# Kernel tuning notes

Hardware: AMD Instinct MI355X
Metric: run time of the kernel (lower is better)

Reference implementation:

```python
import jax, jax.numpy as jnp
import numpy as np

BITS = 4
MAXQ = (1 << BITS) - 1  # 15
PACK = 32 // BITS       # 8 nibbles per int32


def setup_inputs() -> dict:
    key = jax.random.key(0)
    k = jax.random.split(key, 6)
    B, S, IN, OUT, G = 4, 2048, 4096, 4096, 32
    groups = IN // G  # 128
    imin, imax = np.iinfo(np.int32).min, np.iinfo(np.int32).max
    x = jax.random.normal(k[0], (B, S, IN), dtype=jnp.float32)
    qweight = jax.random.randint(k[1], (IN // PACK, OUT), imin, imax, dtype=jnp.int32)
    qzeros = jax.random.randint(k[2], (groups, OUT // PACK), imin, imax, dtype=jnp.int32)
    qscales = jax.random.randint(k[3], (groups, OUT, 1), 0, 256, dtype=jnp.int32)
    qscales_zeros = jax.random.uniform(k[4], (groups, 1, 1), dtype=jnp.float32)
    qscales_scales = jax.random.uniform(k[5], (groups, 1, 1), dtype=jnp.float32) * 0.01
    g_idx = (jnp.arange(IN, dtype=jnp.int32) // G)
    return {"x": x, "qweight": qweight, "qzeros": qzeros, "qscales": qscales,
            "qscales_zeros": qscales_zeros, "qscales_scales": qscales_scales, "g_idx": g_idx}


def reference(x, qweight, qzeros, qscales, qscales_zeros, qscales_scales, g_idx):
    out_features = qweight.shape[-1]
    shifts = jnp.arange(0, 32, BITS, dtype=jnp.int32)  # (8,)
    # --- unpack int4 weights: (in/8, 8, out) -> (in, out); mask makes arith shift == logical
    w = (qweight[:, None, :] >> shifts[None, :, None]) & MAXQ
    w = w.reshape(-1, out_features)  # (in, out), values 0..15
    # --- unpack zeros: (groups, out/8, 8) -> (groups, out); +1 per original
    z = ((qzeros[:, :, None] >> shifts[None, None, :]) & MAXQ) + 1
    z = z.reshape(qzeros.shape[0], -1)  # (groups, out)
    z = z[g_idx]  # (in, out)
    # --- double-dequant scales: (groups, out, 1) with (groups, 1, 1) stats
    scales = (qscales.astype(x.dtype) - qscales_zeros) * qscales_scales
    scales = scales.reshape(qscales.shape[0], -1)[g_idx]  # (in, out)
    weight = ((w - z) * scales).astype(x.dtype)  # (in, out)
    return jnp.matmul(x, weight)
```

## Files before the change

kernel.cpp:

```cpp
#include <hip/hip_runtime.h>

typedef __attribute__((ext_vector_type(8))) short short8;
typedef __attribute__((ext_vector_type(4))) float floatx4;
typedef unsigned int u32;
typedef unsigned short u16;

__device__ __forceinline__ u16 f2bf(float f) {
  u32 u = __float_as_uint(f);
  u += 0x7FFFu + ((u >> 16) & 1u);
  return (u16)(u >> 16);
}

typedef const __attribute__((address_space(1))) u32* gp1_t;
typedef __attribute__((address_space(3))) u32* lp3_t;

__device__ __forceinline__ void gld16(const void* g, void* l) {
  __builtin_amdgcn_global_load_lds((gp1_t)g, (lp3_t)l, 16, 0, 0);
}

__global__ __launch_bounds__(256) void xconv(const float* __restrict__ x,
                                             u16* __restrict__ xb, long long n4) {
  long long i = (long long)blockIdx.x * 256 + threadIdx.x;
  if (i >= n4) return;
  float4 v = ((const float4*)x)[i];
  ushort4 o;
  o.x = f2bf(v.x); o.y = f2bf(v.y); o.z = f2bf(v.z); o.w = f2bf(v.w);
  ((ushort4*)xb)[i] = o;
}

__global__ __launch_bounds__(256) void dequant(
    const int* __restrict__ qw, const int* __restrict__ qz,
    const int* __restrict__ qs, const float* __restrict__ qsz,
    const float* __restrict__ qss, const int* __restrict__ gidx,
    u16* __restrict__ Wt, int IN, int OUT) {
  const int n = blockIdx.x * 64 + (threadIdx.x & 63);
  const int w = threadIdx.x >> 6;
  const int k0 = blockIdx.y * 128 + w * 32;
  const int g = gidx[k0];
  const int kk0 = k0 >> 3;
  const int zq = ((qz[(size_t)g * (OUT >> 3) + (n >> 3)] >> (4 * (n & 7))) & 15) + 1;
  const float sc = ((float)qs[(size_t)g * OUT + n] - qsz[g]) * qss[g];
  u16* dst = Wt + (size_t)n * IN + k0;
#pragma unroll
  for (int j = 0; j < 4; ++j) {
    const int w32 = qw[(size_t)(kk0 + j) * OUT + n];
    u16 o[8];
#pragma unroll
    for (int s = 0; s < 8; ++s)
      o[s] = f2bf((float)(((w32 >> (4 * s)) & 15) - zq) * sc);
    uint4 pk;
    pk.x = (u32)o[0] | ((u32)o[1] << 16);
    pk.y = (u32)o[2] | ((u32)o[3] << 16);
    pk.z = (u32)o[4] | ((u32)o[5] << 16);
    pk.w = (u32)o[6] | ((u32)o[7] << 16);
    *(uint4*)(dst + j * 8) = pk;
  }
}

#define VM4 asm volatile("s_waitcnt vmcnt(4)" ::: "memory")
#define VM0 asm volatile("s_waitcnt vmcnt(0)" ::: "memory")

__global__ __launch_bounds__(512, 2) void gemm256(const u16* __restrict__ A,
                                                  const u16* __restrict__ Bt,
                                                  float* __restrict__ C,
                                                  int M, int N, int K) {
  __shared__ u16 As[2][16384];
  __shared__ u16 Bs[2][16384];
  const int tid = threadIdx.x;
  const int lane = tid & 63;
  const int wave = tid >> 6;
  const int wm = wave >> 2;
  const int wn = wave & 3;
  const int lr = lane & 15, quad = lane >> 4;

  const int nbx = N >> 8;
  const int nwg = gridDim.x;
  const int bid = blockIdx.x;
  const int q8 = nwg >> 3, r8 = nwg & 7;
  const int xcd = bid & 7, loc = bid >> 3;
  const int swz = (xcd < r8 ? xcd * (q8 + 1) : r8 * (q8 + 1) + (xcd - r8) * q8) + loc;
  const int n0 = (swz % nbx) << 8;
  const int m0 = (swz / nbx) << 8;

  floatx4 acc[8][4] = {};

  const int srow = lane >> 3;
  const int sch8 = ((lane & 7) ^ (srow & 7)) * 8;
  const u16* aS = A + (size_t)(m0 + wave * 8 + srow) * K + sch8;
  const u16* bS = Bt + (size_t)(n0 + wave * 8 + srow) * K + sch8;

#define STAGE_A(buf, h, kt) do {                                              \
    const u16* s_ = aS + (size_t)(h) * 128 * K + (size_t)(kt) * 64;           \
    u16* d_ = &As[buf][((h) * 128 + wave * 8) * 64];                          \
    gld16(s_, d_); gld16(s_ + (size_t)64 * K, d_ + 4096);                     \
  } while (0)
#define STAGE_B(buf, h, kt) do {                                              \
    const u16* s_ = bS + (size_t)(h) * 128 * K + (size_t)(kt) * 64;           \
    u16* d_ = &Bs[buf][((h) * 128 + wave * 8) * 64];                          \
    gld16(s_, d_); gld16(s_ + (size_t)64 * K, d_ + 4096);                     \
  } while (0)

  const int rl = lr & 7;
  const int cs0 = ((0 * 4 + quad) ^ rl) * 8;
  const int cs1 = ((1 * 4 + quad) ^ rl) * 8;
  const u16* a0rd = &As[0][(wm * 128 + lr) * 64];
  const u16* a1rd = &As[1][(wm * 128 + lr) * 64];
  const u16* b0rd = &Bs[0][(wn * 64 + lr) * 64];
  const u16* b1rd = &Bs[1][(wn * 64 + lr) * 64];

  short8 aF[2][2], bF[4][2];

#define PHASE(ARD, BRD, q, LOADB, STG, VMW) do {                              \
    if (LOADB) {                                                              \
      _Pragma("unroll") for (int nt = 0; nt < 4; ++nt) {                      \
        bF[nt][0] = *(const short8*)((BRD) + nt * 1024 + cs0);                \
        bF[nt][1] = *(const short8*)((BRD) + nt * 1024 + cs1);                \
      }                                                                       \
    }                                                                         \
    aF[0][0] = *(const short8*)((ARD) + (2 * (q)) * 1024 + cs0);              \
    aF[0][1] = *(const short8*)((ARD) + (2 * (q)) * 1024 + cs1);              \
    aF[1][0] = *(const short8*)((ARD) + (2 * (q) + 1) * 1024 + cs0);          \
    aF[1][1] = *(const short8*)((ARD) + (2 * (q) + 1) * 1024 + cs1);          \
    STG;                                                                      \
    __builtin_amdgcn_s_barrier();                                             \
    __builtin_amdgcn_s_setprio(1);                                            \
    _Pragma("unroll") for (int s = 0; s < 2; ++s)                             \
      _Pragma("unroll") for (int j = 0; j < 2; ++j)                           \
        _Pragma("unroll") for (int nt = 0; nt < 4; ++nt)                      \
          acc[2 * (q) + j][nt] = __builtin_amdgcn_mfma_f32_16x16x32_bf16(     \
              aF[j][s], bF[nt][s], acc[2 * (q) + j][nt], 0, 0, 0);            \
    __builtin_amdgcn_s_setprio(0);                                            \
    VMW;                                                                      \
    __builtin_amdgcn_s_barrier();                                             \
  } while (0)

  STAGE_B(0, 0, 0); STAGE_B(0, 1, 0);
  STAGE_A(0, 0, 0); STAGE_A(0, 1, 0);
  STAGE_B(1, 0, 1); STAGE_B(1, 1, 1);
  VM4;
  __builtin_amdgcn_s_barrier();

  const int NI = K >> 7;
  for (int i = 0; i < NI; ++i) {
    const int kt = 2 * i;
    const bool full = (i < NI - 1);
    PHASE(a0rd, b0rd, 0, 1, { STAGE_A(1, 0, kt + 1); }, (void)0);
    PHASE(a0rd, b0rd, 1, 0, { STAGE_A(1, 1, kt + 1); }, (void)0);
    PHASE(a0rd, b0rd, 2, 0, { if (full) STAGE_B(0, 0, kt + 2); }, (void)0);
    PHASE(a0rd, b0rd, 3, 0, { if (full) STAGE_B(0, 1, kt + 2); },
          { if (full) { VM4; } else { VM0; } });
    PHASE(a1rd, b1rd, 0, 1, { if (full) STAGE_A(0, 0, kt + 2); }, (void)0);
    PHASE(a1rd, b1rd, 1, 0, { if (full) STAGE_A(0, 1, kt + 2); }, (void)0);
    PHASE(a1rd, b1rd, 2, 0, { if (full) STAGE_B(1, 0, kt + 3); }, (void)0);
    PHASE(a1rd, b1rd, 3, 0, { if (full) STAGE_B(1, 1, kt + 3); },
          { if (full) { VM4; } });
  }
#undef PHASE
#undef STAGE_A
#undef STAGE_B

#pragma unroll
  for (int mt = 0; mt < 8; ++mt)
#pragma unroll
    for (int nt = 0; nt < 4; ++nt)
#pragma unroll
      for (int r = 0; r < 4; ++r) {
        int row = m0 + wm * 128 + mt * 16 + quad * 4 + r;
        int col = n0 + wn * 64 + nt * 16 + lr;
        C[(size_t)row * N + col] = acc[mt][nt][r];
      }
}

__global__ __launch_bounds__(256) void gemm(const u16* __restrict__ A,
                                            const u16* __restrict__ Bt,
                                            float* __restrict__ C,
                                            int M, int N, int K) {
  __shared__ u16 As[128 * 64];
  __shared__ u16 Bs[128 * 64];
  const int tid = threadIdx.x;
  const int lane = tid & 63;
  const int wave = tid >> 6;
  const int wm = wave & 1, wn = wave >> 1;
  const int lr = lane & 15, quad = lane >> 4;
  const int m0 = blockIdx.y * 128, n0 = blockIdx.x * 128;

  floatx4 acc[4][4] = {};

  const int srowB = (lane >> 3);
  const int schunk = (lane & 7) ^ srowB;
  const int rowA0 = wave * 32;
  const u16* aSrc = A + (size_t)(m0 + rowA0 + srowB) * K + schunk * 8;
  const u16* bSrc = Bt + (size_t)(n0 + rowA0 + srowB) * K + schunk * 8;
  u16* aDst = &As[rowA0 * 64];
  u16* bDst = &Bs[rowA0 * 64];
  const size_t rstep = (size_t)8 * K;

  const int rx = lr & 7;

  for (int k0 = 0; k0 < K; k0 += 64) {
    __syncthreads();
#pragma unroll
    for (int c = 0; c < 4; ++c) {
      gld16(aSrc + c * rstep + k0, aDst + c * 8 * 64);
      gld16(bSrc + c * rstep + k0, bDst + c * 8 * 64);
    }
    __syncthreads();

#pragma unroll
    for (int h = 0; h < 2; ++h) {
      short8 aF[4], bF[4];
      const int rc = ((quad + 4 * h) ^ rx) * 8;
#pragma unroll
      for (int t = 0; t < 4; ++t) {
        aF[t] = *(const short8*)&As[(wm * 64 + t * 16 + lr) * 64 + rc];
        bF[t] = *(const short8*)&Bs[(wn * 64 + t * 16 + lr) * 64 + rc];
      }
#pragma unroll
      for (int mt = 0; mt < 4; ++mt)
#pragma unroll
        for (int nt = 0; nt < 4; ++nt)
          acc[mt][nt] = __builtin_amdgcn_mfma_f32_16x16x32_bf16(
              aF[mt], bF[nt], acc[mt][nt], 0, 0, 0);
    }
  }

#pragma unroll
  for (int mt = 0; mt < 4; ++mt)
#pragma unroll
    for (int nt = 0; nt < 4; ++nt)
#pragma unroll
      for (int r = 0; r < 4; ++r) {
        int row = m0 + wm * 64 + mt * 16 + quad * 4 + r;
        int col = n0 + wn * 64 + nt * 16 + lr;
        C[(size_t)row * N + col] = acc[mt][nt][r];
      }
}

__global__ void naive(const float* __restrict__ x, const int* __restrict__ qw,
                      const int* __restrict__ qz, const int* __restrict__ qs,
                      const float* __restrict__ qsz, const float* __restrict__ qss,
                      const int* __restrict__ gidx, float* __restrict__ out,
                      int M, int N, int K) {
  int n = blockIdx.x * 64 + (threadIdx.x & 63);
  int m = blockIdx.y * 4 + (threadIdx.x >> 6);
  if (n >= N || m >= M) return;
  float acc = 0.f;
  for (int kk = 0; kk < K / 8; ++kk) {
    int w32 = qw[(size_t)kk * N + n];
#pragma unroll
    for (int s = 0; s < 8; ++s) {
      int k = kk * 8 + s;
      int g = gidx[k];
      int zq = ((qz[(size_t)g * (N >> 3) + (n >> 3)] >> (4 * (n & 7))) & 15) + 1;
      float sc = ((float)qs[(size_t)g * N + n] - qsz[g]) * qss[g];
      acc += x[(size_t)m * K + k] * ((float)((w32 >> (4 * s)) & 15) - (float)zq) * sc;
    }
  }
  out[(size_t)m * N + n] = acc;
}

extern "C" void kernel_launch(void* const* d_in, const int* in_sizes, int n_in,
                              void* d_out, int out_size, void* d_ws, size_t ws_size,
                              hipStream_t stream) {
  const float* x = (const float*)d_in[0];
  const int* qw = (const int*)d_in[1];
  const int* qz = (const int*)d_in[2];
  const int* qs = (const int*)d_in[3];
  const float* qsz = (const float*)d_in[4];
  const float* qss = (const float*)d_in[5];
  const int* gidx = (const int*)d_in[6];
  const int IN = in_sizes[6];
  const int OUT = (int)(((long long)in_sizes[1] * 8) / IN);
  const int M = in_sizes[0] / IN;
  float* out = (float*)d_out;

  size_t bytesW = (size_t)IN * OUT * 2;
  size_t bytesX = (size_t)M * IN * 2;
  bool haveWs = (ws_size >= bytesW + bytesX);
  bool fast256 = haveWs && (M % 256 == 0) && (OUT % 256 == 0) &&
                 (IN % 128 == 0) && (IN >= 256);
  bool fast128 = haveWs && (M % 128 == 0) && (OUT % 128 == 0) && (IN % 128 == 0);

  if (fast256 || fast128) {
    u16* Wt = (u16*)d_ws;
    u16* Xb = (u16*)((char*)d_ws + bytesW);
    long long n4 = (long long)M * IN / 4;
    int cb = (int)((n4 + 255) / 256);
    xconv<<<cb, 256, 0, stream>>>(x, Xb, n4);
    dequant<<<dim3(OUT / 64, IN / 128), 256, 0, stream>>>(qw, qz, qs, qsz, qss,
                                                          gidx, Wt, IN, OUT);
    if (fast256) {
      int nblk = (M / 256) * (OUT / 256);
      gemm256<<<dim3(nblk), 512, 0, stream>>>(Xb, Wt, out, M, OUT, IN);
    } else {
      gemm<<<dim3(OUT / 128, M / 128), 256, 0, stream>>>(Xb, Wt, out, M, OUT, IN);
    }
  } else {
    naive<<<dim3((OUT + 63) / 64, (M + 3) / 4), 256, 0, stream>>>(
        x, qw, qz, qs, qsz, qss, gidx, out, M, OUT, IN);
  }
}
```

Before: 489.8 us.

## Restructure GEMM main loop into two-barrier tiles and coalesce dequant stores via LDS

The GEMM main loop is rewritten from eight single-barrier phases per iteration into per-k-tile blocks. Each block waits on vmcnt once, loads all B and low A fragments, issues the next A stage, runs MFMAs while loading the high A fragments, then barriers and issues the next B stage. This aims to cut barrier count and overlap LDS reads with MFMA, at the cost of more live registers and a peeled epilogue. The dequant kernel now stages its output through shared memory so global stores of the transposed weight are coalesced, and xconv becomes a grid-stride loop capped at 2048 blocks.

```diff
diff --git a/kernel.cpp b/kernel.cpp
--- a/kernel.cpp
+++ b/kernel.cpp
@@ -20,12 +20,13 @@
 
 __global__ __launch_bounds__(256) void xconv(const float* __restrict__ x,
                                              u16* __restrict__ xb, long long n4) {
-  long long i = (long long)blockIdx.x * 256 + threadIdx.x;
-  if (i >= n4) return;
-  float4 v = ((const float4*)x)[i];
-  ushort4 o;
-  o.x = f2bf(v.x); o.y = f2bf(v.y); o.z = f2bf(v.z); o.w = f2bf(v.w);
-  ((ushort4*)xb)[i] = o;
+  const long long stride = (long long)gridDim.x * 256;
+  for (long long i = (long long)blockIdx.x * 256 + threadIdx.x; i < n4; i += stride) {
+    float4 v = ((const float4*)x)[i];
+    ushort4 o;
+    o.x = f2bf(v.x); o.y = f2bf(v.y); o.z = f2bf(v.z); o.w = f2bf(v.w);
+    ((ushort4*)xb)[i] = o;
+  }
 }
 
 __global__ __launch_bounds__(256) void dequant(
@@ -33,27 +34,41 @@
     const int* __restrict__ qs, const float* __restrict__ qsz,
     const float* __restrict__ qss, const int* __restrict__ gidx,
     u16* __restrict__ Wt, int IN, int OUT) {
-  const int n = blockIdx.x * 64 + (threadIdx.x & 63);
-  const int w = threadIdx.x >> 6;
-  const int k0 = blockIdx.y * 128 + w * 32;
-  const int g = gidx[k0];
-  const int kk0 = k0 >> 3;
-  const int zq = ((qz[(size_t)g * (OUT >> 3) + (n >> 3)] >> (4 * (n & 7))) & 15) + 1;
-  const float sc = ((float)qs[(size_t)g * OUT + n] - qsz[g]) * qss[g];
-  u16* dst = Wt + (size_t)n * IN + k0;
-#pragma unroll
-  for (int j = 0; j < 4; ++j) {
-    const int w32 = qw[(size_t)(kk0 + j) * OUT + n];
-    u16 o[8];
-#pragma unroll
-    for (int s = 0; s < 8; ++s)
-      o[s] = f2bf((float)(((w32 >> (4 * s)) & 15) - zq) * sc);
-    uint4 pk;
-    pk.x = (u32)o[0] | ((u32)o[1] << 16);
-    pk.y = (u32)o[2] | ((u32)o[3] << 16);
-    pk.z = (u32)o[4] | ((u32)o[5] << 16);
-    pk.w = (u32)o[6] | ((u32)o[7] << 16);
-    *(uint4*)(dst + j * 8) = pk;
+  __shared__ u16 Lt[64][136];
+  const int t = threadIdx.x;
+  const int n0 = blockIdx.x * 64;
+  const int k0 = blockIdx.y * 128;
+
+  {
+    const int nl = t & 63, kw = t >> 6;
+    const int n = n0 + nl;
+#pragma unroll
+    for (int j = 0; j < 4; ++j) {
+      const int widx = kw + j * 4;
+      const int g = gidx[k0 + widx * 8];
+      const int zq = ((qz[(size_t)g * (OUT >> 3) + (n >> 3)] >> (4 * (n & 7))) & 15) + 1;
+      const float sc = ((float)qs[(size_t)g * OUT + n] - qsz[g]) * qss[g];
+      const int w32 = qw[(size_t)(k0 / 8 + widx) * OUT + n];
+      u16 o[8];
+#pragma unroll
+      for (int s = 0; s < 8; ++s)
+        o[s] = f2bf((float)(((w32 >> (4 * s)) & 15) - zq) * sc);
+      uint4 pk;
+      pk.x = (u32)o[0] | ((u32)o[1] << 16);
+      pk.y = (u32)o[2] | ((u32)o[3] << 16);
+      pk.z = (u32)o[4] | ((u32)o[5] << 16);
+      pk.w = (u32)o[6] | ((u32)o[7] << 16);
+      *(uint4*)&Lt[nl][widx * 8] = pk;
+    }
+  }
+  __syncthreads();
+
+  {
+    const int nl = t >> 2, kq = t & 3;
+    u16* dst = Wt + (size_t)(n0 + nl) * IN + k0 + kq * 32;
+#pragma unroll
+    for (int i = 0; i < 4; ++i)
+      *(uint4*)(dst + i * 8) = *(const uint4*)&Lt[nl][kq * 32 + i * 8];
   }
 }
 
@@ -89,16 +104,18 @@
   const u16* aS = A + (size_t)(m0 + wave * 8 + srow) * K + sch8;
   const u16* bS = Bt + (size_t)(n0 + wave * 8 + srow) * K + sch8;
 
-#define STAGE_A(buf, h, kt) do {                                              \
-    const u16* s_ = aS + (size_t)(h) * 128 * K + (size_t)(kt) * 64;           \
-    u16* d_ = &As[buf][((h) * 128 + wave * 8) * 64];                          \
-    gld16(s_, d_); gld16(s_ + (size_t)64 * K, d_ + 4096);                     \
-  } while (0)
-#define STAGE_B(buf, h, kt) do {                                              \
-    const u16* s_ = bS + (size_t)(h) * 128 * K + (size_t)(kt) * 64;           \
-    u16* d_ = &Bs[buf][((h) * 128 + wave * 8) * 64];                          \
-    gld16(s_, d_); gld16(s_ + (size_t)64 * K, d_ + 4096);                     \
-  } while (0)
+#define STAGE_A(buf, kt) do {                                                 \
+    _Pragma("unroll") for (int h_ = 0; h_ < 2; ++h_) {                        \
+      const u16* s_ = aS + (size_t)h_ * 128 * K + (size_t)(kt) * 64;          \
+      u16* d_ = &As[buf][(h_ * 128 + wave * 8) * 64];                         \
+      gld16(s_, d_); gld16(s_ + (size_t)64 * K, d_ + 4096);                   \
+    } } while (0)
+#define STAGE_B(buf, kt) do {                                                 \
+    _Pragma("unroll") for (int h_ = 0; h_ < 2; ++h_) {                        \
+      const u16* s_ = bS + (size_t)h_ * 128 * K + (size_t)(kt) * 64;          \
+      u16* d_ = &Bs[buf][(h_ * 128 + wave * 8) * 64];                         \
+      gld16(s_, d_); gld16(s_ + (size_t)64 * K, d_ + 4096);                   \
+    } } while (0)
 
   const int rl = lr & 7;
   const int cs0 = ((0 * 4 + quad) ^ rl) * 8;
@@ -108,54 +125,54 @@
   const u16* b0rd = &Bs[0][(wn * 64 + lr) * 64];
   const u16* b1rd = &Bs[1][(wn * 64 + lr) * 64];
 
-  short8 aF[2][2], bF[4][2];
-
-#define PHASE(ARD, BRD, q, LOADB, STG, VMW) do {                              \
-    if (LOADB) {                                                              \
-      _Pragma("unroll") for (int nt = 0; nt < 4; ++nt) {                      \
-        bF[nt][0] = *(const short8*)((BRD) + nt * 1024 + cs0);                \
-        bF[nt][1] = *(const short8*)((BRD) + nt * 1024 + cs1);                \
-      }                                                                       \
-    }                                                                         \
-    aF[0][0] = *(const short8*)((ARD) + (2 * (q)) * 1024 + cs0);              \
-    aF[0][1] = *(const short8*)((ARD) + (2 * (q)) * 1024 + cs1);              \
-    aF[1][0] = *(const short8*)((ARD) + (2 * (q) + 1) * 1024 + cs0);          \
-    aF[1][1] = *(const short8*)((ARD) + (2 * (q) + 1) * 1024 + cs1);          \
-    STG;                                                                      \
-    __builtin_amdgcn_s_barrier();                                             \
+#define MFMA16(JB, AARR)                                                      \
     __builtin_amdgcn_s_setprio(1);                                            \
     _Pragma("unroll") for (int s = 0; s < 2; ++s)                             \
       _Pragma("unroll") for (int j = 0; j < 2; ++j)                           \
         _Pragma("unroll") for (int nt = 0; nt < 4; ++nt)                      \
-          acc[2 * (q) + j][nt] = __builtin_amdgcn_mfma_f32_16x16x32_bf16(     \
-              aF[j][s], bF[nt][s], acc[2 * (q) + j][nt], 0, 0, 0);            \
-    __builtin_amdgcn_s_setprio(0);                                            \
+          acc[(JB) + j][nt] = __builtin_amdgcn_mfma_f32_16x16x32_bf16(        \
+              AARR[((JB) & 2) + j][s], bF[nt][s], acc[(JB) + j][nt], 0, 0, 0);\
+    __builtin_amdgcn_s_setprio(0);
+
+#define TILE(ARD, BRD, STGA, STGB, VMW) do {                                  \
     VMW;                                                                      \
     __builtin_amdgcn_s_barrier();                                             \
+    short8 bF[4][2], aL[4][2], aH[4][2];                                      \
+    _Pragma("unroll") for (int nt = 0; nt < 4; ++nt) {                        \
+      bF[nt][0] = *(const short8*)((BRD) + nt * 1024 + cs0);                  \
+      bF[nt][1] = *(const short8*)((BRD) + nt * 1024 + cs1);                  \
+    }                                                                         \
+    _Pragma("unroll") for (int j = 0; j < 4; ++j) {                           \
+      aL[j][0] = *(const short8*)((ARD) + j * 1024 + cs0);                    \
+      aL[j][1] = *(const short8*)((ARD) + j * 1024 + cs1);                    \
+    }                                                                         \
+    STGA;                                                                     \
+    MFMA16(0, aL)                                                             \
+    _Pragma("unroll") for (int j = 0; j < 4; ++j) {                           \
+      aH[j][0] = *(const short8*)((ARD) + (4 + j) * 1024 + cs0);              \
+      aH[j][1] = *(const short8*)((ARD) + (4 + j) * 1024 + cs1);              \
+    }                                                                         \
+    MFMA16(2, aL)                                                             \
+    __builtin_amdgcn_s_barrier();        \
+    STGB;                                                                     \
+    MFMA16(4, aH)                                                             \
+    MFMA16(6, aH)                                                             \
   } while (0)
 
-  STAGE_B(0, 0, 0); STAGE_B(0, 1, 0);
-  STAGE_A(0, 0, 0); STAGE_A(0, 1, 0);
-  STAGE_B(1, 0, 1); STAGE_B(1, 1, 1);
-  VM4;
-  __builtin_amdgcn_s_barrier();
+  STAGE_B(0, 0);
+  STAGE_A(0, 0);
+  STAGE_B(1, 1);
 
   const int NI = K >> 7;
-  for (int i = 0; i < NI; ++i) {
+  for (int i = 0; i < NI - 1; ++i) {
     const int kt = 2 * i;
-    const bool full = (i < NI - 1);
-    PHASE(a0rd, b0rd, 0, 1, { STAGE_A(1, 0, kt + 1); }, (void)0);
-    PHASE(a0rd, b0rd, 1, 0, { STAGE_A(1, 1, kt + 1); }, (void)0);
-    PHASE(a0rd, b0rd, 2, 0, { if (full) STAGE_B(0, 0, kt + 2); }, (void)0);
-    PHASE(a0rd, b0rd, 3, 0, { if (full) STAGE_B(0, 1, kt + 2); },
-          { if (full) { VM4; } else { VM0; } });
-    PHASE(a1rd, b1rd, 0, 1, { if (full) STAGE_A(0, 0, kt + 2); }, (void)0);
-    PHASE(a1rd, b1rd, 1, 0, { if (full) STAGE_A(0, 1, kt + 2); }, (void)0);
-    PHASE(a1rd, b1rd, 2, 0, { if (full) STAGE_B(1, 0, kt + 3); }, (void)0);
-    PHASE(a1rd, b1rd, 3, 0, { if (full) STAGE_B(1, 1, kt + 3); },
-          { if (full) { VM4; } });
-  }
-#undef PHASE
+    TILE(a0rd, b0rd, { STAGE_A(1, kt + 1); }, { STAGE_B(0, kt + 2); }, VM4);
+    TILE(a1rd, b1rd, { STAGE_A(0, kt + 2); }, { STAGE_B(1, kt + 3); }, VM4);
+  }
+  TILE(a0rd, b0rd, { STAGE_A(1, 2 * NI - 1); }, (void)0, VM4);
+  TILE(a1rd, b1rd, (void)0, (void)0, VM0);
+#undef TILE
+#undef MFMA16
 #undef STAGE_A
 #undef STAGE_B
 
@@ -278,7 +295,7 @@
   size_t bytesX = (size_t)M * IN * 2;
   bool haveWs = (ws_size >= bytesW + bytesX);
   bool fast256 = haveWs && (M % 256 == 0) && (OUT % 256 == 0) &&
-                 (IN % 128 == 0) && (IN >= 256);
+                 (IN % 256 == 0) && (IN >= 256);
   bool fast128 = haveWs && (M % 128 == 0) && (OUT % 128 == 0) && (IN % 128 == 0);
 
   if (fast256 || fast128) {
@@ -286,6 +303,7 @@
     u16* Xb = (u16*)((char*)d_ws + bytesW);
     long long n4 = (long long)M * IN / 4;
     int cb = (int)((n4 + 255) / 256);
+    if (cb > 2048) cb = 2048;
     xconv<<<cb, 256, 0, stream>>>(x, Xb, n4);
     dequant<<<dim3(OUT / 64, IN / 128), 256, 0, stream>>>(qw, qz, qs, qsz, qss,
                                                           gidx, Wt, IN, OUT);
```

After: 475.2 us. -3.0%, faster.
